# Kernel optimization log

Hardware: AMD Instinct MI355X
Metric: run time of the kernel (lower is better)

## Reference

```python
import jax, jax.numpy as jnp
import numpy as np

N_NODES = 100000
N_EDGES = 1600000
IN_CH = 64
HID = 64
N_GRAPHS = 64


def _sage_conv(x, src, dst, Wl, bl, Wr, n_nodes):
    # PyG SAGEConv (aggr='mean'): out = lin_l(mean_{j in N(i)} x_j) + lin_r(x_i)
    msg = x[src]                                            # [E, d] gather
    agg = jax.ops.segment_sum(msg, dst, num_segments=n_nodes)
    cnt = jax.ops.segment_sum(jnp.ones((src.shape[0],), x.dtype), dst,
                              num_segments=n_nodes)
    agg = agg / jnp.maximum(cnt, 1.0)[:, None]
    return agg @ Wl + bl + x @ Wr


def setup_inputs() -> dict:
    key = jax.random.key(0)
    ks = jax.random.split(key, 16)
    x = jax.random.normal(ks[0], (N_NODES, IN_CH), jnp.float32)
    edge_index = jax.random.randint(ks[1], (2, N_EDGES), 0, N_NODES, jnp.int64)
    batch = jnp.sort(jax.random.randint(ks[2], (N_NODES,), 0, N_GRAPHS, jnp.int64))

    def glorot(k, fan_in, fan_out):
        s = jnp.sqrt(2.0 / (fan_in + fan_out))
        return jax.random.normal(k, (fan_in, fan_out), jnp.float32) * s

    params = {
        'W1l': glorot(ks[3], IN_CH, HID), 'b1': jnp.zeros((HID,), jnp.float32),
        'W1r': glorot(ks[4], IN_CH, HID),
        'W2l': glorot(ks[5], HID, HID), 'b2': jnp.zeros((HID,), jnp.float32),
        'W2r': glorot(ks[6], HID, HID),
        'W3l': glorot(ks[7], HID, HID), 'b3': jnp.zeros((HID,), jnp.float32),
        'W3r': glorot(ks[8], HID, HID),
        'Wc1': glorot(ks[9], HID, HID // 2), 'bc1': jnp.zeros((HID // 2,), jnp.float32),
        'Wc2': glorot(ks[10], HID // 2, 2), 'bc2': jnp.zeros((2,), jnp.float32),
    }
    return {'x': x, 'edge_index': edge_index, 'batch': batch, **params}


def reference(x, edge_index, batch,
              W1l, b1, W1r, W2l, b2, W2r, W3l, b3, W3r,
              Wc1, bc1, Wc2, bc2):
    src, dst = edge_index[0], edge_index[1]
    n = x.shape[0]
    h = jax.nn.relu(_sage_conv(x, src, dst, W1l, b1, W1r, n))   # dropout = identity (eval)
    h = jax.nn.relu(_sage_conv(h, src, dst, W2l, b2, W2r, n))
    h = jax.nn.relu(_sage_conv(h, src, dst, W3l, b3, W3r, n))
    # global mean pool over graphs
    sums = jax.ops.segment_sum(h, batch, num_segments=N_GRAPHS)
    cnts = jax.ops.segment_sum(jnp.ones((n,), h.dtype), batch, num_segments=N_GRAPHS)
    g = sums / jnp.maximum(cnts, 1.0)[:, None]                  # [G, HID]
    # MLP head (dropout = identity at eval)
    return jax.nn.relu(g @ Wc1 + bc1) @ Wc2 + bc2               # [G, 2]
```

## Files before the change

kernel.cpp:

```cpp
#include <hip/hip_runtime.h>
#include <hip/hip_bf16.h>
#include <hip/hip_fp16.h>

typedef unsigned int u32;
typedef unsigned short u16;
typedef _Float16 f16x8 __attribute__((ext_vector_type(8)));
typedef float f32x4 __attribute__((ext_vector_type(4)));

#define NBLK1 512
#define MMBLK 256

__device__ __forceinline__ u16 f2h(float f) { return __half_as_ushort(__float2half(f)); }
__device__ __forceinline__ u32 packh2(float a, float b) {
    return (u32)f2h(a) | ((u32)f2h(b) << 16);
}
__device__ __forceinline__ __half2 sx(__half2 v, int m) {
    int iv = __shfl_xor(*(int*)&v, m, 64);
    return *(__half2*)&iv;
}

__device__ __forceinline__ int gidx(const void* p, long long i, int w64) {
    if (w64) return (int)((const long long*)p)[i];
    return ((const int*)p)[i];
}

__device__ __forceinline__ int detect_w64(const int* edge_words, int E, int tid, int* sh) {
    if (tid == 0) *sh = 0;
    __syncthreads();
    const long long totalWords = 2LL * E;
    const long long step = totalWords / 256;
    long long w = ((long long)tid * step) | 1;
    int nz = (w < totalWords) ? edge_words[w] : 0;
    if (nz) atomicOr(sh, 1);
    __syncthreads();
    return (*sh) ? 0 : 1;
}

__global__ void __launch_bounds__(256) fused_hist_mm1(
        const void* __restrict__ edge, int* __restrict__ flag, u32* __restrict__ ticket,
        u32* __restrict__ HG, int E, int n, int nb1,
        const float* __restrict__ X, const float* __restrict__ Wl,
        const float* __restrict__ Wr, const float* __restrict__ Bv,
        u16* __restrict__ Z, u16* __restrict__ R) {
    if (blockIdx.x < NBLK1) {
        __shared__ u32 h[256];
        __shared__ int shnz;
        const int tid = threadIdx.x;
        h[tid] = 0;
        const int w64 = detect_w64((const int*)edge, E, tid, &shnz);
        if (blockIdx.x == 0 && tid == 0) { flag[0] = w64; *ticket = 0; }
        __syncthreads();
        const int chunk = (E + NBLK1 - 1) / NBLK1;
        const int s = blockIdx.x * chunk;
        const int e = min(s + chunk, E);
        for (int i = s + tid; i < e; i += 256) {
            int d = gidx(edge, (long long)E + i, w64);
            if ((unsigned)d >= (unsigned)n) d = 0;
            atomicAdd(&h[d >> 9], 1);
        }
        __syncthreads();
        for (int b = tid; b < nb1; b += 256) HG[b * NBLK1 + blockIdx.x] = h[b];
        return;
    }
    const int lane = threadIdx.x & 63;
    const int quad = lane >> 4;
    const int m16 = lane & 15;
    f16x8 bl[2][4], br[2][4];
#pragma unroll
    for (int kh = 0; kh < 2; ++kh)
#pragma unroll
        for (int t = 0; t < 4; ++t)
#pragma unroll
            for (int j = 0; j < 8; ++j) {
                int k = kh * 32 + quad * 8 + j;
                int c = t * 16 + m16;
                bl[kh][t][j] = (_Float16)Wl[k * 64 + c];
                br[kh][t][j] = (_Float16)Wr[k * 64 + c];
            }
    float bias_t[4];
#pragma unroll
    for (int t = 0; t < 4; ++t) bias_t[t] = Bv[t * 16 + m16];

    const int ntiles = (n + 15) >> 4;
    const int nwaves = (gridDim.x - NBLK1) * 4;
    for (int tile = (blockIdx.x - NBLK1) * 4 + (threadIdx.x >> 6); tile < ntiles; tile += nwaves) {
        const int nodeBase = tile << 4;
        int nodeA = nodeBase + m16;
        if (nodeA >= n) nodeA = n - 1;
        f16x8 a[2];
#pragma unroll
        for (int kh = 0; kh < 2; ++kh) {
            const float4* p = (const float4*)(X + (size_t)nodeA * 64 + kh * 32 + quad * 8);
            float4 x0 = p[0], x1 = p[1];
            a[kh][0] = (_Float16)x0.x; a[kh][1] = (_Float16)x0.y;
            a[kh][2] = (_Float16)x0.z; a[kh][3] = (_Float16)x0.w;
            a[kh][4] = (_Float16)x1.x; a[kh][5] = (_Float16)x1.y;
            a[kh][6] = (_Float16)x1.z; a[kh][7] = (_Float16)x1.w;
        }
        f32x4 cl[4], cr[4];
#pragma unroll
        for (int t = 0; t < 4; ++t) {
            f32x4 c0 = {0.f, 0.f, 0.f, 0.f};
            c0 = __builtin_amdgcn_mfma_f32_16x16x32_f16(a[0], bl[0][t], c0, 0, 0, 0);
            c0 = __builtin_amdgcn_mfma_f32_16x16x32_f16(a[1], bl[1][t], c0, 0, 0, 0);
            cl[t] = c0;
            f32x4 c1 = {0.f, 0.f, 0.f, 0.f};
            c1 = __builtin_amdgcn_mfma_f32_16x16x32_f16(a[0], br[0][t], c1, 0, 0, 0);
            c1 = __builtin_amdgcn_mfma_f32_16x16x32_f16(a[1], br[1][t], c1, 0, 0, 0);
            cr[t] = c1;
        }
#pragma unroll
        for (int rg = 0; rg < 4; ++rg) {
            const int node = nodeBase + quad * 4 + rg;
            if (node < n) {
#pragma unroll
                for (int t = 0; t < 4; ++t) {
                    const int c = t * 16 + m16;
                    Z[(size_t)node * 64 + c] = f2h(cl[t][rg]);
                    R[(size_t)node * 64 + c] = f2h(cr[t][rg] + bias_t[t]);
                }
            }
        }
    }
}

__global__ void scanAB(u32* __restrict__ HG, u32* __restrict__ blockSums,
                       u32* __restrict__ SB, u32* __restrict__ ticket, int n) {
    __shared__ u32 ts[256];
    __shared__ int isLast;
    const int ITEMS = 8;
    const int tid = threadIdx.x;
    int base = blockIdx.x * 2048 + tid * ITEMS;
    u32 v[ITEMS];
    u32 sum = 0;
#pragma unroll
    for (int i = 0; i < ITEMS; ++i) {
        int idx = base + i;
        v[i] = (idx < n) ? HG[idx] : 0;
        sum += v[i];
    }
    ts[tid] = sum;
    __syncthreads();
    u32 incl = sum;
    for (int d = 1; d < 256; d <<= 1) {
        u32 y = 0;
        if (tid >= d) y = ts[tid - d];
        __syncthreads();
        incl += y;
        ts[tid] = incl;
        __syncthreads();
    }
    u32 run = incl - sum;
#pragma unroll
    for (int i = 0; i < ITEMS; ++i) {
        int idx = base + i;
        if (idx < n) HG[idx] = run;
        run += v[i];
    }
    if (tid == 255) {
        atomicExch(&blockSums[blockIdx.x], incl);
        __threadfence();
        u32 t = atomicAdd(ticket, 1);
        isLast = (t == gridDim.x - 1);
    }
    __syncthreads();
    if (!isLast) return;
    const int nb = gridDim.x;
    u32 bv = (tid < nb) ? atomicAdd(&blockSums[tid], 0u) : 0;
    ts[tid] = bv;
    __syncthreads();
    u32 bincl = bv;
    for (int d = 1; d < 256; d <<= 1) {
        u32 y = 0;
        if (tid >= d) y = ts[tid - d];
        __syncthreads();
        bincl += y;
        ts[tid] = bincl;
        __syncthreads();
    }
    if (tid < nb) SB[tid] = bincl - bv;
}

__global__ void __launch_bounds__(256) p1_scatter(const void* __restrict__ edge,
                                                  const int* __restrict__ flag,
                                                  const u32* __restrict__ HG,
                                                  const u32* __restrict__ SB,
                                                  u32* __restrict__ P, int E, int n, int nb1) {
    __shared__ u32 base[256];
    __shared__ u32 cur[256];
    const int tid = threadIdx.x;
    cur[tid] = 0;
    for (int b = tid; b < nb1; b += 256) {
        int i = b * NBLK1 + blockIdx.x;
        base[b] = HG[i] + SB[i >> 11];
    }
    __syncthreads();
    const int w64 = flag[0];
    const int chunk = (E + NBLK1 - 1) / NBLK1;
    const int s = blockIdx.x * chunk;
    const int e = min(s + chunk, E);
    for (int i = s + tid; i < e; i += 256) {
        int d = gidx(edge, (long long)E + i, w64);
        if ((unsigned)d >= (unsigned)n) d = 0;
        int sv = gidx(edge, i, w64);
        if ((unsigned)sv >= (unsigned)n) sv = 0;
        const int b1 = d >> 9;
        u32 r = atomicAdd(&cur[b1], 1);
        P[base[b1] + r] = (u32)sv | ((u32)(d & 511) << 17);
    }
}

__global__ void __launch_bounds__(256) p2_kernel(const u32* __restrict__ P,
                                                 const u32* __restrict__ HG,
                                                 const u32* __restrict__ SB,
                                                 u32* __restrict__ offs,
                                                 int* __restrict__ ss,
                                                 float* __restrict__ pool,
                                                 int E, int n, int nb1) {
    __shared__ u32 h2[512];
    __shared__ u32 ts[256];
    const int tid = threadIdx.x;
    const int b = blockIdx.x;
    if (b == 0)
        for (int i = tid; i < 4096; i += 256) pool[i] = 0.f;
    const int i0 = b * NBLK1;
    const int bs = (int)(HG[i0] + SB[i0 >> 11]);
    int be;
    if (b + 1 < nb1) {
        const int i1 = (b + 1) * NBLK1;
        be = (int)(HG[i1] + SB[i1 >> 11]);
    } else be = E;
    h2[tid] = 0;
    h2[tid + 256] = 0;
    __syncthreads();
    for (int i = bs + tid; i < be; i += 256) atomicAdd(&h2[(P[i] >> 17) & 511], 1);
    __syncthreads();
    u32 v0 = h2[2 * tid], v1 = h2[2 * tid + 1];
    u32 sum = v0 + v1;
    ts[tid] = sum;
    __syncthreads();
    u32 incl = sum;
    for (int d = 1; d < 256; d <<= 1) {
        u32 y = 0;
        if (tid >= d) y = ts[tid - d];
        __syncthreads();
        incl += y;
        ts[tid] = incl;
        __syncthreads();
    }
    u32 run = incl - sum;
    h2[2 * tid] = run;
    h2[2 * tid + 1] = run + v0;
    const int node0 = b * 512 + 2 * tid;
    if (node0 < n) offs[node0] = bs + run;
    if (node0 + 1 < n) offs[node0 + 1] = bs + run + v0;
    if (b == 0 && tid == 0) offs[n] = (u32)E;
    __syncthreads();
    for (int i = bs + tid; i < be; i += 256) {
        u32 p = P[i];
        u32 r = atomicAdd(&h2[(p >> 17) & 511], 1);
        ss[bs + r] = (int)(p & 0x1FFFFu);
    }
}

__global__ void __launch_bounds__(256) mm_mfma_kernel(const u16* __restrict__ X,
                                                      const float* __restrict__ Wl,
                                                      const float* __restrict__ Wr,
                                                      const float* __restrict__ Bv,
                                                      u16* __restrict__ Z,
                                                      u16* __restrict__ R, int n) {
    const int lane = threadIdx.x & 63;
    const int quad = lane >> 4;
    const int m16 = lane & 15;
    f16x8 bl[2][4], br[2][4];
#pragma unroll
    for (int kh = 0; kh < 2; ++kh)
#pragma unroll
        for (int t = 0; t < 4; ++t)
#pragma unroll
            for (int j = 0; j < 8; ++j) {
                int k = kh * 32 + quad * 8 + j;
                int c = t * 16 + m16;
                bl[kh][t][j] = (_Float16)Wl[k * 64 + c];
                br[kh][t][j] = (_Float16)Wr[k * 64 + c];
            }
    float bias_t[4];
#pragma unroll
    for (int t = 0; t < 4; ++t) bias_t[t] = Bv[t * 16 + m16];

    const int ntiles = (n + 15) >> 4;
    const int nwaves = gridDim.x * 4;
    for (int tile = blockIdx.x * 4 + (threadIdx.x >> 6); tile < ntiles; tile += nwaves) {
        const int nodeBase = tile << 4;
        int nodeA = nodeBase + m16;
        if (nodeA >= n) nodeA = n - 1;
        const _Float16* xp = (const _Float16*)X + (size_t)nodeA * 64;
        f16x8 a[2];
#pragma unroll
        for (int kh = 0; kh < 2; ++kh)
            a[kh] = *(const f16x8*)(xp + kh * 32 + quad * 8);
        f32x4 cl[4], cr[4];
#pragma unroll
        for (int t = 0; t < 4; ++t) {
            f32x4 c0 = {0.f, 0.f, 0.f, 0.f};
            c0 = __builtin_amdgcn_mfma_f32_16x16x32_f16(a[0], bl[0][t], c0, 0, 0, 0);
            c0 = __builtin_amdgcn_mfma_f32_16x16x32_f16(a[1], bl[1][t], c0, 0, 0, 0);
            cl[t] = c0;
            f32x4 c1 = {0.f, 0.f, 0.f, 0.f};
            c1 = __builtin_amdgcn_mfma_f32_16x16x32_f16(a[0], br[0][t], c1, 0, 0, 0);
            c1 = __builtin_amdgcn_mfma_f32_16x16x32_f16(a[1], br[1][t], c1, 0, 0, 0);
            cr[t] = c1;
        }
#pragma unroll
        for (int rg = 0; rg < 4; ++rg) {
            const int node = nodeBase + quad * 4 + rg;
            if (node < n) {
#pragma unroll
                for (int t = 0; t < 4; ++t) {
                    const int c = t * 16 + m16;
                    Z[(size_t)node * 64 + c] = f2h(cl[t][rg]);
                    R[(size_t)node * 64 + c] = f2h(cr[t][rg] + bias_t[t]);
                }
            }
        }
    }
}

__global__ void __launch_bounds__(256) agg_kernel(const u16* __restrict__ Zin,
                                                  const u16* __restrict__ Rin,
                                                  const u32* __restrict__ offs,
                                                  const int* __restrict__ ss,
                                                  u16* __restrict__ Hout, int n) {
    const int lane = threadIdx.x & 63;
    const int q = lane >> 4;
    const int sub = lane & 15;
    const u32* Z32 = (const u32*)Zin;
    const int node = (blockIdx.x << 2) | (threadIdx.x >> 6);
    if (node >= n) return;
    const int off = (int)offs[node], end = (int)offs[node + 1];
    const int deg = end - off;
    const __half2 zero2 = __float2half2_rn(0.f);
    const __half2 one2 = __float2half2_rn(1.f);
    __half2 a0 = zero2, a1 = zero2, b0 = zero2, b1 = zero2;
    __half2 c0 = zero2, c1 = zero2, d0 = zero2, d1 = zero2;
    for (int base = off; base < end; base += 64) {
        const int cnt = min(64, end - base);
        const int idx = ss[base + (lane < cnt ? lane : cnt - 1)];
        int p = 0;
        for (; p + 16 <= cnt; p += 16) {
            int j0 = p + q;
            int s0 = __shfl(idx, j0, 64);
            int s1 = __shfl(idx, j0 + 4, 64);
            int s2 = __shfl(idx, j0 + 8, 64);
            int s3 = __shfl(idx, j0 + 12, 64);
            uint2 u0 = *(const uint2*)(Z32 + s0 * 32 + 2 * sub);
            uint2 u1 = *(const uint2*)(Z32 + s1 * 32 + 2 * sub);
            uint2 u2 = *(const uint2*)(Z32 + s2 * 32 + 2 * sub);
            uint2 u3 = *(const uint2*)(Z32 + s3 * 32 + 2 * sub);
            a0 = __hadd2(a0, *(const __half2*)&u0.x);
            a1 = __hadd2(a1, *(const __half2*)&u0.y);
            b0 = __hadd2(b0, *(const __half2*)&u1.x);
            b1 = __hadd2(b1, *(const __half2*)&u1.y);
            c0 = __hadd2(c0, *(const __half2*)&u2.x);
            c1 = __hadd2(c1, *(const __half2*)&u2.y);
            d0 = __hadd2(d0, *(const __half2*)&u3.x);
            d1 = __hadd2(d1, *(const __half2*)&u3.y);
        }
        const int rem = cnt - p;
        if (rem) {
            int j = p + q, j1 = p + 4 + q;
            int s0 = __shfl(idx, j < cnt ? j : cnt - 1, 64);
            int s1 = __shfl(idx, j1 < cnt ? j1 : cnt - 1, 64);
            uint2 u0 = *(const uint2*)(Z32 + s0 * 32 + 2 * sub);
            uint2 u1 = *(const uint2*)(Z32 + s1 * 32 + 2 * sub);
            __half2 m0 = (j < cnt) ? one2 : zero2;
            __half2 m1 = (j1 < cnt) ? one2 : zero2;
            a0 = __hfma2(*(const __half2*)&u0.x, m0, a0);
            a1 = __hfma2(*(const __half2*)&u0.y, m0, a1);
            b0 = __hfma2(*(const __half2*)&u1.x, m1, b0);
            b1 = __hfma2(*(const __half2*)&u1.y, m1, b1);
            if (rem > 8) {
                int j2 = p + 8 + q, j3 = p + 12 + q;
                int s2 = __shfl(idx, j2 < cnt ? j2 : cnt - 1, 64);
                int s3 = __shfl(idx, j3 < cnt ? j3 : cnt - 1, 64);
                uint2 u2 = *(const uint2*)(Z32 + s2 * 32 + 2 * sub);
                uint2 u3 = *(const uint2*)(Z32 + s3 * 32 + 2 * sub);
                __half2 m2 = (j2 < cnt) ? one2 : zero2;
                __half2 m3 = (j3 < cnt) ? one2 : zero2;
                c0 = __hfma2(*(const __half2*)&u2.x, m2, c0);
                c1 = __hfma2(*(const __half2*)&u2.y, m2, c1);
                d0 = __hfma2(*(const __half2*)&u3.x, m3, d0);
                d1 = __hfma2(*(const __half2*)&u3.y, m3, d1);
            }
        }
    }
    a0 = __hadd2(__hadd2(a0, b0), __hadd2(c0, d0));
    a1 = __hadd2(__hadd2(a1, b1), __hadd2(c1, d1));
    a0 = __hadd2(a0, sx(a0, 16)); a0 = __hadd2(a0, sx(a0, 32));
    a1 = __hadd2(a1, sx(a1, 16)); a1 = __hadd2(a1, sx(a1, 32));
    if (q == 0) {
        const u32* R32 = (const u32*)Rin;
        uint2 rr = *(const uint2*)(R32 + node * 32 + 2 * sub);
        const float rd = deg > 0 ? 1.f / (float)deg : 0.f;
        float2 s01 = __half22float2(a0);
        float2 s23 = __half22float2(a1);
        float2 r01 = __half22float2(*(const __half2*)&rr.x);
        float2 r23 = __half22float2(*(const __half2*)&rr.y);
        uint2 outp;
        outp.x = packh2(fmaxf(fmaf(s01.x, rd, r01.x), 0.f),
                        fmaxf(fmaf(s01.y, rd, r01.y), 0.f));
        outp.y = packh2(fmaxf(fmaf(s23.x, rd, r23.x), 0.f),
                        fmaxf(fmaf(s23.y, rd, r23.y), 0.f));
        *(uint2*)(((u32*)Hout) + node * 32 + 2 * sub) = outp;
    }
}

__global__ void pool_kernel(const u16* __restrict__ H, const void* __restrict__ batch,
                            const int* __restrict__ flag, float* __restrict__ pool, int n) {
    const int lane = threadIdx.x & 63;
    const int wave = threadIdx.x >> 6;
    int start = (blockIdx.x * 4 + wave) * 64;
    int end = min(start + 64, n);
    if (start >= end) return;
    const int w64 = flag[0];
    float acc = 0.f;
    int cur = gidx(batch, start, w64) & 63;
    for (int i = start; i < end; ++i) {
        int g = gidx(batch, i, w64) & 63;
        if (g != cur) {
            atomicAdd(&pool[cur * 64 + lane], acc);
            acc = 0.f;
            cur = g;
        }
        acc += __half2float(__ushort_as_half(H[i * 64 + lane]));
    }
    atomicAdd(&pool[cur * 64 + lane], acc);
}

__global__ void head_kernel(const float* __restrict__ pool, const void* __restrict__ batch,
                            const int* __restrict__ flag,
                            const float* __restrict__ Wc1, const float* __restrict__ bc1,
                            const float* __restrict__ Wc2, const float* __restrict__ bc2,
                            float* __restrict__ out, int n) {
    __shared__ float gm[64 * 64];
    __shared__ float am[64 * 32];
    __shared__ int cnts[64];
    const int tid = threadIdx.x;
    const int w64 = flag[0];
    if (tid < 64) {
        int lo = 0, hi = n;
        while (lo < hi) { int mid = (lo + hi) >> 1; if (gidx(batch, mid, w64) < tid) lo = mid + 1; else hi = mid; }
        int lo2 = 0, hi2 = n;
        int v2 = tid + 1;
        while (lo2 < hi2) { int mid = (lo2 + hi2) >> 1; if (gidx(batch, mid, w64) < v2) lo2 = mid + 1; else hi2 = mid; }
        cnts[tid] = lo2 - lo;
    }
    __syncthreads();
    for (int i = tid; i < 4096; i += 256) {
        int g = i >> 6;
        float c = (float)(cnts[g] > 0 ? cnts[g] : 1);
        gm[i] = pool[i] / c;
    }
    __syncthreads();
    for (int i = tid; i < 64 * 32; i += 256) {
        int g = i >> 5, j = i & 31;
        float acc = bc1[j];
        for (int k = 0; k < 64; ++k) acc += gm[g * 64 + k] * Wc1[k * 32 + j];
        am[i] = acc > 0.f ? acc : 0.f;
    }
    __syncthreads();
    if (tid < 128) {
        int g = tid >> 1, o = tid & 1;
        float acc = bc2[o];
        for (int j = 0; j < 32; ++j) acc += am[g * 32 + j] * Wc2[j * 2 + o];
        out[tid] = acc;
    }
}

extern "C" void kernel_launch(void* const* d_in, const int* in_sizes, int n_in,
                              void* d_out, int out_size, void* d_ws, size_t ws_size,
                              hipStream_t stream) {
    const float* x   = (const float*)d_in[0];
    const void* edge = d_in[1];
    const void* batch = d_in[2];
    const float* W1l = (const float*)d_in[3];
    const float* b1  = (const float*)d_in[4];
    const float* W1r = (const float*)d_in[5];
    const float* W2l = (const float*)d_in[6];
    const float* b2  = (const float*)d_in[7];
    const float* W2r = (const float*)d_in[8];
    const float* W3l = (const float*)d_in[9];
    const float* b3  = (const float*)d_in[10];
    const float* W3r = (const float*)d_in[11];
    const float* Wc1 = (const float*)d_in[12];
    const float* bc1 = (const float*)d_in[13];
    const float* Wc2 = (const float*)d_in[14];
    const float* bc2 = (const float*)d_in[15];

    const int n = in_sizes[0] / 64;
    const int E = in_sizes[1] / 2;
    const int nb1 = (n + 511) >> 9;
    const int NS = nb1 * NBLK1;

    char* w = (char*)d_ws;
    size_t o = 0;
    auto take = [&](size_t bytes) -> void* {
        void* p = w + o;
        o = (o + bytes + 511) & ~(size_t)511;
        return p;
    };
    int* flag      = (int*)take(sizeof(int));
    u32* ticket    = (u32*)take(sizeof(u32));
    u32* offs      = (u32*)take((size_t)(n + 1) * sizeof(u32));
    u32* HG        = (u32*)take((size_t)(NS + 1) * sizeof(u32));
    u32* blockSums = (u32*)take(256 * sizeof(u32));
    u32* SB        = (u32*)take(256 * sizeof(u32));
    u32* P         = (u32*)take((size_t)E * sizeof(u32));
    int* ss        = (int*)take((size_t)E * sizeof(int));
    u16* Z         = (u16*)take((size_t)n * 64 * sizeof(u16));
    u16* R         = (u16*)take((size_t)n * 64 * sizeof(u16));
    u16* HA        = (u16*)take((size_t)n * 64 * sizeof(u16));
    u16* HB        = (u16*)take((size_t)n * 64 * sizeof(u16));
    float* pool    = (float*)take(64 * 64 * sizeof(float));

    fused_hist_mm1<<<NBLK1 + MMBLK, 256, 0, stream>>>(edge, flag, ticket, HG, E, n, nb1,
                                                      x, W1l, W1r, b1, Z, R);
    const int nbScan = (NS + 2047) / 2048;
    scanAB<<<nbScan, 256, 0, stream>>>(HG, blockSums, SB, ticket, NS);
    p1_scatter<<<NBLK1, 256, 0, stream>>>(edge, flag, HG, SB, P, E, n, nb1);
    p2_kernel<<<nb1, 256, 0, stream>>>(P, HG, SB, offs, ss, pool, E, n, nb1);

    const int nodeBlocks = (n + 3) / 4;
    agg_kernel<<<nodeBlocks, 256, 0, stream>>>(Z, R, offs, ss, HA, n);
    mm_mfma_kernel<<<MMBLK, 256, 0, stream>>>(HA, W2l, W2r, b2, Z, R, n);
    agg_kernel<<<nodeBlocks, 256, 0, stream>>>(Z, R, offs, ss, HB, n);
    mm_mfma_kernel<<<MMBLK, 256, 0, stream>>>(HB, W3l, W3r, b3, Z, R, n);
    agg_kernel<<<nodeBlocks, 256, 0, stream>>>(Z, R, offs, ss, HA, n);

    pool_kernel<<<(n + 255) / 256, 256, 0, stream>>>(HA, batch, flag, pool, n);
    head_kernel<<<1, 256, 0, stream>>>(pool, batch, flag, Wc1, bc1, Wc2, bc2,
                                       (float*)d_out, n);
}
```

Baseline: 334.6 us.

## Fuse neighbor aggregation with next layer's MFMA transform per 16-node tile

Aggregation for layers 1 and 2 is merged with the following layer's dense transform into one kernel, aggmm_kernel. Each block aggregates 16 nodes into LDS, then one wave runs MFMA on the tile and writes the next Z/R. The intermediate H buffer's write and read-back and two kernel launches go away, and ping-pong Z/R buffers avoid read-after-write hazards. In exchange, every block reloads and converts the weights, and only one of four waves does the matmul, which may hurt occupancy and balance.

```diff
diff --git a/kernel.cpp b/kernel.cpp
--- a/kernel.cpp
+++ b/kernel.cpp
@@ -36,307 +36,11 @@
     return (*sh) ? 0 : 1;
 }
 
-__global__ void __launch_bounds__(256) fused_hist_mm1(
-        const void* __restrict__ edge, int* __restrict__ flag, u32* __restrict__ ticket,
-        u32* __restrict__ HG, int E, int n, int nb1,
-        const float* __restrict__ X, const float* __restrict__ Wl,
-        const float* __restrict__ Wr, const float* __restrict__ Bv,
-        u16* __restrict__ Z, u16* __restrict__ R) {
-    if (blockIdx.x < NBLK1) {
-        __shared__ u32 h[256];
-        __shared__ int shnz;
-        const int tid = threadIdx.x;
-        h[tid] = 0;
-        const int w64 = detect_w64((const int*)edge, E, tid, &shnz);
-        if (blockIdx.x == 0 && tid == 0) { flag[0] = w64; *ticket = 0; }
-        __syncthreads();
-        const int chunk = (E + NBLK1 - 1) / NBLK1;
-        const int s = blockIdx.x * chunk;
-        const int e = min(s + chunk, E);
-        for (int i = s + tid; i < e; i += 256) {
-            int d = gidx(edge, (long long)E + i, w64);
-            if ((unsigned)d >= (unsigned)n) d = 0;
-            atomicAdd(&h[d >> 9], 1);
-        }
-        __syncthreads();
-        for (int b = tid; b < nb1; b += 256) HG[b * NBLK1 + blockIdx.x] = h[b];
-        return;
-    }
-    const int lane = threadIdx.x & 63;
-    const int quad = lane >> 4;
-    const int m16 = lane & 15;
-    f16x8 bl[2][4], br[2][4];
-#pragma unroll
-    for (int kh = 0; kh < 2; ++kh)
-#pragma unroll
-        for (int t = 0; t < 4; ++t)
-#pragma unroll
-            for (int j = 0; j < 8; ++j) {
-                int k = kh * 32 + quad * 8 + j;
-                int c = t * 16 + m16;
-                bl[kh][t][j] = (_Float16)Wl[k * 64 + c];
-                br[kh][t][j] = (_Float16)Wr[k * 64 + c];
-            }
-    float bias_t[4];
-#pragma unroll
-    for (int t = 0; t < 4; ++t) bias_t[t] = Bv[t * 16 + m16];
-
-    const int ntiles = (n + 15) >> 4;
-    const int nwaves = (gridDim.x - NBLK1) * 4;
-    for (int tile = (blockIdx.x - NBLK1) * 4 + (threadIdx.x >> 6); tile < ntiles; tile += nwaves) {
-        const int nodeBase = tile << 4;
-        int nodeA = nodeBase + m16;
-        if (nodeA >= n) nodeA = n - 1;
-        f16x8 a[2];
-#pragma unroll
-        for (int kh = 0; kh < 2; ++kh) {
-            const float4* p = (const float4*)(X + (size_t)nodeA * 64 + kh * 32 + quad * 8);
-            float4 x0 = p[0], x1 = p[1];
-            a[kh][0] = (_Float16)x0.x; a[kh][1] = (_Float16)x0.y;
-            a[kh][2] = (_Float16)x0.z; a[kh][3] = (_Float16)x0.w;
-            a[kh][4] = (_Float16)x1.x; a[kh][5] = (_Float16)x1.y;
-            a[kh][6] = (_Float16)x1.z; a[kh][7] = (_Float16)x1.w;
-        }
-        f32x4 cl[4], cr[4];
-#pragma unroll
-        for (int t = 0; t < 4; ++t) {
-            f32x4 c0 = {0.f, 0.f, 0.f, 0.f};
-            c0 = __builtin_amdgcn_mfma_f32_16x16x32_f16(a[0], bl[0][t], c0, 0, 0, 0);
-            c0 = __builtin_amdgcn_mfma_f32_16x16x32_f16(a[1], bl[1][t], c0, 0, 0, 0);
-            cl[t] = c0;
-            f32x4 c1 = {0.f, 0.f, 0.f, 0.f};
-            c1 = __builtin_amdgcn_mfma_f32_16x16x32_f16(a[0], br[0][t], c1, 0, 0, 0);
-            c1 = __builtin_amdgcn_mfma_f32_16x16x32_f16(a[1], br[1][t], c1, 0, 0, 0);
-            cr[t] = c1;
-        }
-#pragma unroll
-        for (int rg = 0; rg < 4; ++rg) {
-            const int node = nodeBase + quad * 4 + rg;
-            if (node < n) {
-#pragma unroll
-                for (int t = 0; t < 4; ++t) {
-                    const int c = t * 16 + m16;
-                    Z[(size_t)node * 64 + c] = f2h(cl[t][rg]);
-                    R[(size_t)node * 64 + c] = f2h(cr[t][rg] + bias_t[t]);
-                }
-            }
-        }
-    }
-}
-
-__global__ void scanAB(u32* __restrict__ HG, u32* __restrict__ blockSums,
-                       u32* __restrict__ SB, u32* __restrict__ ticket, int n) {
-    __shared__ u32 ts[256];
-    __shared__ int isLast;
-    const int ITEMS = 8;
-    const int tid = threadIdx.x;
-    int base = blockIdx.x * 2048 + tid * ITEMS;
-    u32 v[ITEMS];
-    u32 sum = 0;
-#pragma unroll
-    for (int i = 0; i < ITEMS; ++i) {
-        int idx = base + i;
-        v[i] = (idx < n) ? HG[idx] : 0;
-        sum += v[i];
-    }
-    ts[tid] = sum;
-    __syncthreads();
-    u32 incl = sum;
-    for (int d = 1; d < 256; d <<= 1) {
-        u32 y = 0;
-        if (tid >= d) y = ts[tid - d];
-        __syncthreads();
-        incl += y;
-        ts[tid] = incl;
-        __syncthreads();
-    }
-    u32 run = incl - sum;
-#pragma unroll
-    for (int i = 0; i < ITEMS; ++i) {
-        int idx = base + i;
-        if (idx < n) HG[idx] = run;
-        run += v[i];
-    }
-    if (tid == 255) {
-        atomicExch(&blockSums[blockIdx.x], incl);
-        __threadfence();
-        u32 t = atomicAdd(ticket, 1);
-        isLast = (t == gridDim.x - 1);
-    }
-    __syncthreads();
-    if (!isLast) return;
-    const int nb = gridDim.x;
-    u32 bv = (tid < nb) ? atomicAdd(&blockSums[tid], 0u) : 0;
-    ts[tid] = bv;
-    __syncthreads();
-    u32 bincl = bv;
-    for (int d = 1; d < 256; d <<= 1) {
-        u32 y = 0;
-        if (tid >= d) y = ts[tid - d];
-        __syncthreads();
-        bincl += y;
-        ts[tid] = bincl;
-        __syncthreads();
-    }
-    if (tid < nb) SB[tid] = bincl - bv;
-}
-
-__global__ void __launch_bounds__(256) p1_scatter(const void* __restrict__ edge,
-                                                  const int* __restrict__ flag,
-                                                  const u32* __restrict__ HG,
-                                                  const u32* __restrict__ SB,
-                                                  u32* __restrict__ P, int E, int n, int nb1) {
-    __shared__ u32 base[256];
-    __shared__ u32 cur[256];
-    const int tid = threadIdx.x;
-    cur[tid] = 0;
-    for (int b = tid; b < nb1; b += 256) {
-        int i = b * NBLK1 + blockIdx.x;
-        base[b] = HG[i] + SB[i >> 11];
-    }
-    __syncthreads();
-    const int w64 = flag[0];
-    const int chunk = (E + NBLK1 - 1) / NBLK1;
-    const int s = blockIdx.x * chunk;
-    const int e = min(s + chunk, E);
-    for (int i = s + tid; i < e; i += 256) {
-        int d = gidx(edge, (long long)E + i, w64);
-        if ((unsigned)d >= (unsigned)n) d = 0;
-        int sv = gidx(edge, i, w64);
-        if ((unsigned)sv >= (unsigned)n) sv = 0;
-        const int b1 = d >> 9;
-        u32 r = atomicAdd(&cur[b1], 1);
-        P[base[b1] + r] = (u32)sv | ((u32)(d & 511) << 17);
-    }
-}
-
-__global__ void __launch_bounds__(256) p2_kernel(const u32* __restrict__ P,
-                                                 const u32* __restrict__ HG,
-                                                 const u32* __restrict__ SB,
-                                                 u32* __restrict__ offs,
-                                                 int* __restrict__ ss,
-                                                 float* __restrict__ pool,
-                                                 int E, int n, int nb1) {
-    __shared__ u32 h2[512];
-    __shared__ u32 ts[256];
-    const int tid = threadIdx.x;
-    const int b = blockIdx.x;
-    if (b == 0)
-        for (int i = tid; i < 4096; i += 256) pool[i] = 0.f;
-    const int i0 = b * NBLK1;
-    const int bs = (int)(HG[i0] + SB[i0 >> 11]);
-    int be;
-    if (b + 1 < nb1) {
-        const int i1 = (b + 1) * NBLK1;
-        be = (int)(HG[i1] + SB[i1 >> 11]);
-    } else be = E;
-    h2[tid] = 0;
-    h2[tid + 256] = 0;
-    __syncthreads();
-    for (int i = bs + tid; i < be; i += 256) atomicAdd(&h2[(P[i] >> 17) & 511], 1);
-    __syncthreads();
-    u32 v0 = h2[2 * tid], v1 = h2[2 * tid + 1];
-    u32 sum = v0 + v1;
-    ts[tid] = sum;
-    __syncthreads();
-    u32 incl = sum;
-    for (int d = 1; d < 256; d <<= 1) {
-        u32 y = 0;
-        if (tid >= d) y = ts[tid - d];
-        __syncthreads();
-        incl += y;
-        ts[tid] = incl;
-        __syncthreads();
-    }
-    u32 run = incl - sum;
-    h2[2 * tid] = run;
-    h2[2 * tid + 1] = run + v0;
-    const int node0 = b * 512 + 2 * tid;
-    if (node0 < n) offs[node0] = bs + run;
-    if (node0 + 1 < n) offs[node0 + 1] = bs + run + v0;
-    if (b == 0 && tid == 0) offs[n] = (u32)E;
-    __syncthreads();
-    for (int i = bs + tid; i < be; i += 256) {
-        u32 p = P[i];
-        u32 r = atomicAdd(&h2[(p >> 17) & 511], 1);
-        ss[bs + r] = (int)(p & 0x1FFFFu);
-    }
-}
-
-__global__ void __launch_bounds__(256) mm_mfma_kernel(const u16* __restrict__ X,
-                                                      const float* __restrict__ Wl,
-                                                      const float* __restrict__ Wr,
-                                                      const float* __restrict__ Bv,
-                                                      u16* __restrict__ Z,
-                                                      u16* __restrict__ R, int n) {
-    const int lane = threadIdx.x & 63;
-    const int quad = lane >> 4;
-    const int m16 = lane & 15;
-    f16x8 bl[2][4], br[2][4];
-#pragma unroll
-    for (int kh = 0; kh < 2; ++kh)
-#pragma unroll
-        for (int t = 0; t < 4; ++t)
-#pragma unroll
-            for (int j = 0; j < 8; ++j) {
-                int k = kh * 32 + quad * 8 + j;
-                int c = t * 16 + m16;
-                bl[kh][t][j] = (_Float16)Wl[k * 64 + c];
-                br[kh][t][j] = (_Float16)Wr[k * 64 + c];
-            }
-    float bias_t[4];
-#pragma unroll
-    for (int t = 0; t < 4; ++t) bias_t[t] = Bv[t * 16 + m16];
-
-    const int ntiles = (n + 15) >> 4;
-    const int nwaves = gridDim.x * 4;
-    for (int tile = blockIdx.x * 4 + (threadIdx.x >> 6); tile < ntiles; tile += nwaves) {
-        const int nodeBase = tile << 4;
-        int nodeA = nodeBase + m16;
-        if (nodeA >= n) nodeA = n - 1;
-        const _Float16* xp = (const _Float16*)X + (size_t)nodeA * 64;
-        f16x8 a[2];
-#pragma unroll
-        for (int kh = 0; kh < 2; ++kh)
-            a[kh] = *(const f16x8*)(xp + kh * 32 + quad * 8);
-        f32x4 cl[4], cr[4];
-#pragma unroll
-        for (int t = 0; t < 4; ++t) {
-            f32x4 c0 = {0.f, 0.f, 0.f, 0.f};
-            c0 = __builtin_amdgcn_mfma_f32_16x16x32_f16(a[0], bl[0][t], c0, 0, 0, 0);
-            c0 = __builtin_amdgcn_mfma_f32_16x16x32_f16(a[1], bl[1][t], c0, 0, 0, 0);
-            cl[t] = c0;
-            f32x4 c1 = {0.f, 0.f, 0.f, 0.f};
-            c1 = __builtin_amdgcn_mfma_f32_16x16x32_f16(a[0], br[0][t], c1, 0, 0, 0);
-            c1 = __builtin_amdgcn_mfma_f32_16x16x32_f16(a[1], br[1][t], c1, 0, 0, 0);
-            cr[t] = c1;
-        }
-#pragma unroll
-        for (int rg = 0; rg < 4; ++rg) {
-            const int node = nodeBase + quad * 4 + rg;
-            if (node < n) {
-#pragma unroll
-                for (int t = 0; t < 4; ++t) {
-                    const int c = t * 16 + m16;
-                    Z[(size_t)node * 64 + c] = f2h(cl[t][rg]);
-                    R[(size_t)node * 64 + c] = f2h(cr[t][rg] + bias_t[t]);
-                }
-            }
-        }
-    }
-}
-
-__global__ void __launch_bounds__(256) agg_kernel(const u16* __restrict__ Zin,
-                                                  const u16* __restrict__ Rin,
-                                                  const u32* __restrict__ offs,
-                                                  const int* __restrict__ ss,
-                                                  u16* __restrict__ Hout, int n) {
-    const int lane = threadIdx.x & 63;
-    const int q = lane >> 4;
-    const int sub = lane & 15;
-    const u32* Z32 = (const u32*)Zin;
-    const int node = (blockIdx.x << 2) | (threadIdx.x >> 6);
-    if (node >= n) return;
+__device__ __forceinline__ uint2 agg_node(const u32* __restrict__ Z32,
+                                          const u32* __restrict__ R32,
+                                          const u32* __restrict__ offs,
+                                          const int* __restrict__ ss,
+                                          int node, int lane, int q, int sub) {
     const int off = (int)offs[node], end = (int)offs[node + 1];
     const int deg = end - off;
     const __half2 zero2 = __float2half2_rn(0.f);
@@ -398,21 +102,334 @@
     a1 = __hadd2(__hadd2(a1, b1), __hadd2(c1, d1));
     a0 = __hadd2(a0, sx(a0, 16)); a0 = __hadd2(a0, sx(a0, 32));
     a1 = __hadd2(a1, sx(a1, 16)); a1 = __hadd2(a1, sx(a1, 32));
-    if (q == 0) {
-        const u32* R32 = (const u32*)Rin;
-        uint2 rr = *(const uint2*)(R32 + node * 32 + 2 * sub);
-        const float rd = deg > 0 ? 1.f / (float)deg : 0.f;
-        float2 s01 = __half22float2(a0);
-        float2 s23 = __half22float2(a1);
-        float2 r01 = __half22float2(*(const __half2*)&rr.x);
-        float2 r23 = __half22float2(*(const __half2*)&rr.y);
-        uint2 outp;
-        outp.x = packh2(fmaxf(fmaf(s01.x, rd, r01.x), 0.f),
-                        fmaxf(fmaf(s01.y, rd, r01.y), 0.f));
-        outp.y = packh2(fmaxf(fmaf(s23.x, rd, r23.x), 0.f),
-                        fmaxf(fmaf(s23.y, rd, r23.y), 0.f));
+    uint2 rr = *(const uint2*)(R32 + node * 32 + 2 * sub);
+    const float rd = deg > 0 ? 1.f / (float)deg : 0.f;
+    float2 s01 = __half22float2(a0);
+    float2 s23 = __half22float2(a1);
+    float2 r01 = __half22float2(*(const __half2*)&rr.x);
+    float2 r23 = __half22float2(*(const __half2*)&rr.y);
+    uint2 outp;
+    outp.x = packh2(fmaxf(fmaf(s01.x, rd, r01.x), 0.f),
+                    fmaxf(fmaf(s01.y, rd, r01.y), 0.f));
+    outp.y = packh2(fmaxf(fmaf(s23.x, rd, r23.x), 0.f),
+                    fmaxf(fmaf(s23.y, rd, r23.y), 0.f));
+    return outp;
+}
+
+__global__ void __launch_bounds__(256) fused_hist_mm1(
+        const void* __restrict__ edge, int* __restrict__ flag, u32* __restrict__ ticket,
+        u32* __restrict__ HG, int E, int n, int nb1,
+        const float* __restrict__ X, const float* __restrict__ Wl,
+        const float* __restrict__ Wr, const float* __restrict__ Bv,
+        u16* __restrict__ Z, u16* __restrict__ R) {
+    if (blockIdx.x < NBLK1) {
+        __shared__ u32 h[256];
+        __shared__ int shnz;
+        const int tid = threadIdx.x;
+        h[tid] = 0;
+        const int w64 = detect_w64((const int*)edge, E, tid, &shnz);
+        if (blockIdx.x == 0 && tid == 0) { flag[0] = w64; *ticket = 0; }
+        __syncthreads();
+        const int chunk = (E + NBLK1 - 1) / NBLK1;
+        const int s = blockIdx.x * chunk;
+        const int e = min(s + chunk, E);
+        for (int i = s + tid; i < e; i += 256) {
+            int d = gidx(edge, (long long)E + i, w64);
+            if ((unsigned)d >= (unsigned)n) d = 0;
+            atomicAdd(&h[d >> 9], 1);
+        }
+        __syncthreads();
+        for (int b = tid; b < nb1; b += 256) HG[b * NBLK1 + blockIdx.x] = h[b];
+        return;
+    }
+    const int lane = threadIdx.x & 63;
+    const int quad = lane >> 4;
+    const int m16 = lane & 15;
+    f16x8 bl[2][4], br[2][4];
+#pragma unroll
+    for (int kh = 0; kh < 2; ++kh)
+#pragma unroll
+        for (int t = 0; t < 4; ++t)
+#pragma unroll
+            for (int j = 0; j < 8; ++j) {
+                int k = kh * 32 + quad * 8 + j;
+                int c = t * 16 + m16;
+                bl[kh][t][j] = (_Float16)Wl[k * 64 + c];
+                br[kh][t][j] = (_Float16)Wr[k * 64 + c];
+            }
+    float bias_t[4];
+#pragma unroll
+    for (int t = 0; t < 4; ++t) bias_t[t] = Bv[t * 16 + m16];
+
+    const int ntiles = (n + 15) >> 4;
+    const int nwaves = (gridDim.x - NBLK1) * 4;
+    for (int tile = (blockIdx.x - NBLK1) * 4 + (threadIdx.x >> 6); tile < ntiles; tile += nwaves) {
+        const int nodeBase = tile << 4;
+        int nodeA = nodeBase + m16;
+        if (nodeA >= n) nodeA = n - 1;
+        f16x8 a[2];
+#pragma unroll
+        for (int kh = 0; kh < 2; ++kh) {
+            const float4* p = (const float4*)(X + (size_t)nodeA * 64 + kh * 32 + quad * 8);
+            float4 x0 = p[0], x1 = p[1];
+            a[kh][0] = (_Float16)x0.x; a[kh][1] = (_Float16)x0.y;
+            a[kh][2] = (_Float16)x0.z; a[kh][3] = (_Float16)x0.w;
+            a[kh][4] = (_Float16)x1.x; a[kh][5] = (_Float16)x1.y;
+            a[kh][6] = (_Float16)x1.z; a[kh][7] = (_Float16)x1.w;
+        }
+        f32x4 cl[4], cr[4];
+#pragma unroll
+        for (int t = 0; t < 4; ++t) {
+            f32x4 c0 = {0.f, 0.f, 0.f, 0.f};
+            c0 = __builtin_amdgcn_mfma_f32_16x16x32_f16(a[0], bl[0][t], c0, 0, 0, 0);
+            c0 = __builtin_amdgcn_mfma_f32_16x16x32_f16(a[1], bl[1][t], c0, 0, 0, 0);
+            cl[t] = c0;
+            f32x4 c1 = {0.f, 0.f, 0.f, 0.f};
+            c1 = __builtin_amdgcn_mfma_f32_16x16x32_f16(a[0], br[0][t], c1, 0, 0, 0);
+            c1 = __builtin_amdgcn_mfma_f32_16x16x32_f16(a[1], br[1][t], c1, 0, 0, 0);
+            cr[t] = c1;
+        }
+#pragma unroll
+        for (int rg = 0; rg < 4; ++rg) {
+            const int node = nodeBase + quad * 4 + rg;
+            if (node < n) {
+#pragma unroll
+                for (int t = 0; t < 4; ++t) {
+                    const int c = t * 16 + m16;
+                    Z[(size_t)node * 64 + c] = f2h(cl[t][rg]);
+                    R[(size_t)node * 64 + c] = f2h(cr[t][rg] + bias_t[t]);
+                }
+            }
+        }
+    }
+}
+
+__global__ void scanAB(u32* __restrict__ HG, u32* __restrict__ blockSums,
+                       u32* __restrict__ SB, u32* __restrict__ ticket, int n) {
+    __shared__ u32 ts[256];
+    __shared__ int isLast;
+    const int ITEMS = 8;
+    const int tid = threadIdx.x;
+    int base = blockIdx.x * 2048 + tid * ITEMS;
+    u32 v[ITEMS];
+    u32 sum = 0;
+#pragma unroll
+    for (int i = 0; i < ITEMS; ++i) {
+        int idx = base + i;
+        v[i] = (idx < n) ? HG[idx] : 0;
+        sum += v[i];
+    }
+    ts[tid] = sum;
+    __syncthreads();
+    u32 incl = sum;
+    for (int d = 1; d < 256; d <<= 1) {
+        u32 y = 0;
+        if (tid >= d) y = ts[tid - d];
+        __syncthreads();
+        incl += y;
+        ts[tid] = incl;
+        __syncthreads();
+    }
+    u32 run = incl - sum;
+#pragma unroll
+    for (int i = 0; i < ITEMS; ++i) {
+        int idx = base + i;
+        if (idx < n) HG[idx] = run;
+        run += v[i];
+    }
+    if (tid == 255) {
+        atomicExch(&blockSums[blockIdx.x], incl);
+        __threadfence();
+        u32 t = atomicAdd(ticket, 1);
+        isLast = (t == gridDim.x - 1);
+    }
+    __syncthreads();
+    if (!isLast) return;
+    const int nb = gridDim.x;
+    u32 bv = (tid < nb) ? atomicAdd(&blockSums[tid], 0u) : 0;
+    ts[tid] = bv;
+    __syncthreads();
+    u32 bincl = bv;
+    for (int d = 1; d < 256; d <<= 1) {
+        u32 y = 0;
+        if (tid >= d) y = ts[tid - d];
+        __syncthreads();
+        bincl += y;
+        ts[tid] = bincl;
+        __syncthreads();
+    }
+    if (tid < nb) SB[tid] = bincl - bv;
+}
+
+__global__ void __launch_bounds__(256) p1_scatter(const void* __restrict__ edge,
+                                                  const int* __restrict__ flag,
+                                                  const u32* __restrict__ HG,
+                                                  const u32* __restrict__ SB,
+                                                  u32* __restrict__ P, int E, int n, int nb1) {
+    __shared__ u32 base[256];
+    __shared__ u32 cur[256];
+    const int tid = threadIdx.x;
+    cur[tid] = 0;
+    for (int b = tid; b < nb1; b += 256) {
+        int i = b * NBLK1 + blockIdx.x;
+        base[b] = HG[i] + SB[i >> 11];
+    }
+    __syncthreads();
+    const int w64 = flag[0];
+    const int chunk = (E + NBLK1 - 1) / NBLK1;
+    const int s = blockIdx.x * chunk;
+    const int e = min(s + chunk, E);
+    for (int i = s + tid; i < e; i += 256) {
+        int d = gidx(edge, (long long)E + i, w64);
+        if ((unsigned)d >= (unsigned)n) d = 0;
+        int sv = gidx(edge, i, w64);
+        if ((unsigned)sv >= (unsigned)n) sv = 0;
+        const int b1 = d >> 9;
+        u32 r = atomicAdd(&cur[b1], 1);
+        P[base[b1] + r] = (u32)sv | ((u32)(d & 511) << 17);
+    }
+}
+
+__global__ void __launch_bounds__(256) p2_kernel(const u32* __restrict__ P,
+                                                 const u32* __restrict__ HG,
+                                                 const u32* __restrict__ SB,
+                                                 u32* __restrict__ offs,
+                                                 int* __restrict__ ss,
+                                                 float* __restrict__ pool,
+                                                 int E, int n, int nb1) {
+    __shared__ u32 h2[512];
+    __shared__ u32 ts[256];
+    const int tid = threadIdx.x;
+    const int b = blockIdx.x;
+    if (b == 0)
+        for (int i = tid; i < 4096; i += 256) pool[i] = 0.f;
+    const int i0 = b * NBLK1;
+    const int bs = (int)(HG[i0] + SB[i0 >> 11]);
+    int be;
+    if (b + 1 < nb1) {
+        const int i1 = (b + 1) * NBLK1;
+        be = (int)(HG[i1] + SB[i1 >> 11]);
+    } else be = E;
+    h2[tid] = 0;
+    h2[tid + 256] = 0;
+    __syncthreads();
+    for (int i = bs + tid; i < be; i += 256) atomicAdd(&h2[(P[i] >> 17) & 511], 1);
+    __syncthreads();
+    u32 v0 = h2[2 * tid], v1 = h2[2 * tid + 1];
+    u32 sum = v0 + v1;
+    ts[tid] = sum;
+    __syncthreads();
+    u32 incl = sum;
+    for (int d = 1; d < 256; d <<= 1) {
+        u32 y = 0;
+        if (tid >= d) y = ts[tid - d];
+        __syncthreads();
+        incl += y;
+        ts[tid] = incl;
+        __syncthreads();
+    }
+    u32 run = incl - sum;
+    h2[2 * tid] = run;
+    h2[2 * tid + 1] = run + v0;
+    const int node0 = b * 512 + 2 * tid;
+    if (node0 < n) offs[node0] = bs + run;
+    if (node0 + 1 < n) offs[node0 + 1] = bs + run + v0;
+    if (b == 0 && tid == 0) offs[n] = (u32)E;
+    __syncthreads();
+    for (int i = bs + tid; i < be; i += 256) {
+        u32 p = P[i];
+        u32 r = atomicAdd(&h2[(p >> 17) & 511], 1);
+        ss[bs + r] = (int)(p & 0x1FFFFu);
+    }
+}
+
+__global__ void __launch_bounds__(256) aggmm_kernel(const u16* __restrict__ Zin,
+                                                    const u16* __restrict__ Rin,
+                                                    const u32* __restrict__ offs,
+                                                    const int* __restrict__ ss,
+                                                    const float* __restrict__ Wl,
+                                                    const float* __restrict__ Wr,
+                                                    const float* __restrict__ Bv,
+                                                    u16* __restrict__ Zout,
+                                                    u16* __restrict__ Rout, int n) {
+    __shared__ u32 hl[16 * 40];
+    const int tid = threadIdx.x;
+    const int lane = tid & 63, wave = tid >> 6;
+    const int q = lane >> 4, sub = lane & 15;
+    const u32* Z32 = (const u32*)Zin;
+    const u32* R32 = (const u32*)Rin;
+    const int nodeBase = blockIdx.x << 4;
+#pragma unroll
+    for (int i = 0; i < 4; ++i) {
+        int node = nodeBase + wave * 4 + i;
+        int nd = node < n ? node : n - 1;
+        uint2 outp = agg_node(Z32, R32, offs, ss, nd, lane, q, sub);
+        if (q == 0) {
+            hl[(wave * 4 + i) * 40 + 2 * sub] = outp.x;
+            hl[(wave * 4 + i) * 40 + 2 * sub + 1] = outp.y;
+        }
+    }
+    __syncthreads();
+    if (wave != 0) return;
+    const int quad = q;
+    const int m16 = lane & 15;
+    f16x8 bl[2][4], br[2][4];
+#pragma unroll
+    for (int kh = 0; kh < 2; ++kh)
+#pragma unroll
+        for (int t = 0; t < 4; ++t)
+#pragma unroll
+            for (int j = 0; j < 8; ++j) {
+                int k = kh * 32 + quad * 8 + j;
+                int c = t * 16 + m16;
+                bl[kh][t][j] = (_Float16)Wl[k * 64 + c];
+                br[kh][t][j] = (_Float16)Wr[k * 64 + c];
+            }
+    float bias_t[4];
+#pragma unroll
+    for (int t = 0; t < 4; ++t) bias_t[t] = Bv[t * 16 + m16];
+    const _Float16* hl16 = (const _Float16*)hl;
+    f16x8 a[2];
+    a[0] = *(const f16x8*)(hl16 + m16 * 80 + quad * 8);
+    a[1] = *(const f16x8*)(hl16 + m16 * 80 + 32 + quad * 8);
+    f32x4 cl[4], cr[4];
+#pragma unroll
+    for (int t = 0; t < 4; ++t) {
+        f32x4 c0 = {0.f, 0.f, 0.f, 0.f};
+        c0 = __builtin_amdgcn_mfma_f32_16x16x32_f16(a[0], bl[0][t], c0, 0, 0, 0);
+        c0 = __builtin_amdgcn_mfma_f32_16x16x32_f16(a[1], bl[1][t], c0, 0, 0, 0);
+        cl[t] = c0;
+        f32x4 c1 = {0.f, 0.f, 0.f, 0.f};
+        c1 = __builtin_amdgcn_mfma_f32_16x16x32_f16(a[0], br[0][t], c1, 0, 0, 0);
+        c1 = __builtin_amdgcn_mfma_f32_16x16x32_f16(a[1], br[1][t], c1, 0, 0, 0);
+        cr[t] = c1;
+    }
+#pragma unroll
+    for (int rg = 0; rg < 4; ++rg) {
+        const int node = nodeBase + quad * 4 + rg;
+        if (node < n) {
+#pragma unroll
+            for (int t = 0; t < 4; ++t) {
+                const int c = t * 16 + m16;
+                Zout[(size_t)node * 64 + c] = f2h(cl[t][rg]);
+                Rout[(size_t)node * 64 + c] = f2h(cr[t][rg] + bias_t[t]);
+            }
+        }
+    }
+}
+
+__global__ void __launch_bounds__(256) agg_kernel(const u16* __restrict__ Zin,
+                                                  const u16* __restrict__ Rin,
+                                                  const u32* __restrict__ offs,
+                                                  const int* __restrict__ ss,
+                                                  u16* __restrict__ Hout, int n) {
+    const int lane = threadIdx.x & 63;
+    const int q = lane >> 4, sub = lane & 15;
+    const int node = (blockIdx.x << 2) | (threadIdx.x >> 6);
+    if (node >= n) return;
+    uint2 outp = agg_node((const u32*)Zin, (const u32*)Rin, offs, ss, node, lane, q, sub);
+    if (q == 0)
         *(uint2*)(((u32*)Hout) + node * 32 + 2 * sub) = outp;
-    }
 }
 
 __global__ void pool_kernel(const u16* __restrict__ H, const void* __restrict__ batch,
@@ -517,25 +534,24 @@
     u32* SB        = (u32*)take(256 * sizeof(u32));
     u32* P         = (u32*)take((size_t)E * sizeof(u32));
     int* ss        = (int*)take((size_t)E * sizeof(int));
-    u16* Z         = (u16*)take((size_t)n * 64 * sizeof(u16));
-    u16* R         = (u16*)take((size_t)n * 64 * sizeof(u16));
+    u16* ZA        = (u16*)take((size_t)n * 64 * sizeof(u16));
+    u16* RA        = (u16*)take((size_t)n * 64 * sizeof(u16));
+    u16* ZB        = (u16*)take((size_t)n * 64 * sizeof(u16));
+    u16* RB        = (u16*)take((size_t)n * 64 * sizeof(u16));
     u16* HA        = (u16*)take((size_t)n * 64 * sizeof(u16));
-    u16* HB        = (u16*)take((size_t)n * 64 * sizeof(u16));
     float* pool    = (float*)take(64 * 64 * sizeof(float));
 
     fused_hist_mm1<<<NBLK1 + MMBLK, 256, 0, stream>>>(edge, flag, ticket, HG, E, n, nb1,
-                                                      x, W1l, W1r, b1, Z, R);
+                                                      x, W1l, W1r, b1, ZA, RA);
     const int nbScan = (NS + 2047) / 2048;
     scanAB<<<nbScan, 256, 0, stream>>>(HG, blockSums, SB, ticket, NS);
     p1_scatter<<<NBLK1, 256, 0, stream>>>(edge, flag, HG, SB, P, E, n, nb1);
     p2_kernel<<<nb1, 256, 0, stream>>>(P, HG, SB, offs, ss, pool, E, n, nb1);
 
-    const int nodeBlocks = (n + 3) / 4;
-    agg_kernel<<<nodeBlocks, 256, 0, stream>>>(Z, R, offs, ss, HA, n);
-    mm_mfma_kernel<<<MMBLK, 256, 0, stream>>>(HA, W2l, W2r, b2, Z, R, n);
-    agg_kernel<<<nodeBlocks, 256, 0, stream>>>(Z, R, offs, ss, HB, n);
-    mm_mfma_kernel<<<MMBLK, 256, 0, stream>>>(HB, W3l, W3r, b3, Z, R, n);
-    agg_kernel<<<nodeBlocks, 256, 0, stream>>>(Z, R, offs, ss, HA, n);
+    const int tileBlocks = (n + 15) / 16;
+    aggmm_kernel<<<tileBlocks, 256, 0, stream>>>(ZA, RA, offs, ss, W2l, W2r, b2, ZB, RB, n);
+    aggmm_kernel<<<tileBlocks, 256, 0, stream>>>(ZB, RB, offs, ss, W3l, W3r, b3, ZA, RA, n);
+    agg_kernel<<<(n + 3) / 4, 256, 0, stream>>>(ZA, RA, offs, ss, HA, n);
 
     pool_kernel<<<(n + 255) / 256, 256, 0, stream>>>(HA, batch, flag, pool, n);
     head_kernel<<<1, 256, 0, stream>>>(pool, batch, flag, Wc1, bc1, Wc2, bc2,
```

Result: slower. 346.4 us (+3.5%).
